# Performance work log

Measured on AMD Instinct MI355X. Metric: run time of the kernel, lower is better.

The kernel has to match this reference:

```python
import jax, jax.numpy as jnp
import numpy as np

R, N, E, IN_DIM, HID, SEM_H = 3, 50000, 500000, 256, 128, 128


def setup_inputs() -> dict:
    key = jax.random.key(0)
    ks = jax.random.split(key, 20)
    s = 0.05
    return {
        # forward tensor args
        "dst_feat": jax.random.normal(ks[0], (N, IN_DIM), jnp.float32),
        "src_feats": jax.random.normal(ks[1], (R, N, IN_DIM), jnp.float32),
        "src_idx": jax.random.randint(ks[2], (R, E), 0, N, jnp.int32),
        "dst_idx": jax.random.randint(ks[3], (R, E), 0, N, jnp.int32),
        # weight_T: per-ntype projection in_dim -> hidden (dst ntype + R src ntypes, stacked)
        "WT_dst": jax.random.normal(ks[4], (IN_DIM, HID), jnp.float32) * s,
        "bT_dst": jnp.zeros((HID,), jnp.float32),
        "WT_src": jax.random.normal(ks[5], (R, IN_DIM, HID), jnp.float32) * s,
        "bT_src": jnp.zeros((R, HID), jnp.float32),
        # GATConv params per relation (1 head, shared fc for src/dst since in_feats is int)
        "W_gat": jax.random.normal(ks[6], (R, HID, HID), jnp.float32) * s,
        "attn_l": jax.random.normal(ks[7], (R, HID), jnp.float32) * s,
        "attn_r": jax.random.normal(ks[8], (R, HID), jnp.float32) * s,
        "b_gat": jnp.zeros((R, HID), jnp.float32),
        # SemanticAttention: Linear(HID,128)+tanh+Linear(128,1,no bias)
        "W1_sem": jax.random.normal(ks[9], (HID, SEM_H), jnp.float32) * s,
        "b1_sem": jnp.zeros((SEM_H,), jnp.float32),
        "w2_sem": jax.random.normal(ks[10], (SEM_H, 1), jnp.float32) * s,
    }


def reference(dst_feat, src_feats, src_idx, dst_idx,
              WT_dst, bT_dst, WT_src, bT_src,
              W_gat, attn_l, attn_r, b_gat,
              W1_sem, b1_sem, w2_sem):
    # weight_T projections (raw feat dim != hidden_dim branch)
    h_dst = dst_feat @ WT_dst + bT_dst                                  # [N, H]
    h_src = jnp.einsum('rni,rio->rno', src_feats, WT_src) + bT_src[:, None, :]  # [R, N, H]
    n_nodes = h_dst.shape[0]

    def gat(h_s_in, si, di, W, al, ar, b):
        # DGL GATConv, 1 head, eval mode (no dropout), shared fc for src/dst
        hs = h_s_in @ W                                                 # [N, H]
        hd = h_dst @ W                                                  # [N, H]
        el = (hs * al).sum(-1)                                          # [N]
        er = (hd * ar).sum(-1)                                          # [N]
        e = el[si] + er[di]                                             # [E]
        e = jnp.where(e > 0, e, 0.2 * e)                                # leaky_relu(0.2)
        # edge softmax segmented by destination node
        m = jax.ops.segment_max(e, di, num_segments=n_nodes)
        ex = jnp.exp(e - m[di])
        ssum = jax.ops.segment_sum(ex, di, num_segments=n_nodes)
        alpha = ex / ssum[di]                                           # [E]
        out = jax.ops.segment_sum(alpha[:, None] * hs[si], di, num_segments=n_nodes)  # [N, H]
        return jax.nn.elu(out + b)                                      # activation=F.elu, + bias

    z_r = jax.vmap(gat)(h_src, src_idx, dst_idx, W_gat, attn_l, attn_r, b_gat)  # [R, N, H]

    # SemanticAttention over relations
    z_m = jnp.transpose(z_r, (1, 0, 2))                                 # [N, R, H]
    w = jnp.tanh(z_m @ W1_sem + b1_sem) @ w2_sem                        # [N, R, 1]
    a = jax.nn.softmax(w.mean(axis=0), axis=0)                          # [R, 1]
    return (z_m * a).sum(axis=1)                                        # [N, H]
```

## Files before the change

kernel.cpp:

```cpp
#include <hip/hip_runtime.h>
#include <hip/hip_bf16.h>

#define R_REL 3
#define NODE_CHUNK 512
#define BCAP 6144

typedef __attribute__((ext_vector_type(8))) short bf16x8;
typedef __attribute__((ext_vector_type(4))) float f32x4;

static inline size_t align_up(size_t x, size_t a) { return (x + a - 1) & ~(a - 1); }

__device__ __forceinline__ float eluf(float x) {
    return x > 0.f ? x : (__expf(x) - 1.f);
}
__device__ __forceinline__ unsigned short f2bf(float f) {
    __hip_bfloat16 h = __float2bfloat16(f);
    return *reinterpret_cast<unsigned short*>(&h);
}
__device__ __forceinline__ unsigned pk2bf(float lo, float hi) {
    __hip_bfloat162 h = __float22bfloat162_rn(make_float2(lo, hi));
    return *reinterpret_cast<unsigned*>(&h);
}
__device__ __forceinline__ float bf2f(unsigned short h) {
    return __uint_as_float((unsigned)h << 16);
}


__global__ void vu_kernel(const float* __restrict__ W_gat, const float* __restrict__ attn_r,
                          const float* __restrict__ WT_dst, const float* __restrict__ bT_dst,
                          float* __restrict__ u, float* __restrict__ cc) {
    int r = blockIdx.x;
    int t = threadIdx.x;
    __shared__ float ar[128];
    __shared__ float vs[128];
    if (t < 128) ar[t] = attn_r[r * 128 + t];
    __syncthreads();
    if (t < 128) {
        const float* W = W_gat + (size_t)r * 128 * 128 + (size_t)t * 128;
        float s = 0.f;
        for (int j = 0; j < 128; ++j) s += W[j] * ar[j];
        vs[t] = s;
    }
    __syncthreads();
    const float* W = WT_dst + (size_t)t * 128;
    float s = 0.f;
    for (int i = 0; i < 128; ++i) s += W[i] * vs[i];
    u[r * 256 + t] = s;
    if (t == 0) {
        float c = 0.f;
        for (int i = 0; i < 128; ++i) c += bT_dst[i] * vs[i];
        cc[r] = c;
    }
}

__global__ void wc_kernel(const float* __restrict__ WT_src, const float* __restrict__ bT_src,
                          const float* __restrict__ W_gat, float* __restrict__ Wc,
                          float* __restrict__ bc) {
    int r = blockIdx.y;
    int k = blockIdx.x;
    int j = threadIdx.x;
    __shared__ float as[128];
    const float* arow = (k < 256) ? (WT_src + ((size_t)r * 256 + k) * 128)
                                  : (bT_src + (size_t)r * 128);
    as[j] = arow[j];
    __syncthreads();
    const float* W = W_gat + (size_t)r * 128 * 128;
    float s = 0.f;
    for (int i = 0; i < 128; ++i) s += as[i] * W[(size_t)i * 128 + j];
    if (k < 256) Wc[((size_t)r * 256 + k) * 128 + j] = s;
    else         bc[(size_t)r * 128 + j] = s;
}

__global__ void pack_kernel(const float* __restrict__ S, unsigned short* __restrict__ P,
                            int relstride, int KS) {
    int r = blockIdx.y;
    int ks = blockIdx.x >> 3, cb = blockIdx.x & 7;
    int l = threadIdx.x;
    const float* Sr = S + (size_t)r * relstride;
    int col = cb * 16 + (l & 15);
    int kb = ks * 32 + (l >> 4) * 8;
    unsigned short v[8];
#pragma unroll
    for (int j = 0; j < 8; ++j) v[j] = f2bf(Sr[(size_t)(kb + j) * 128 + col]);
    unsigned short* dst = P + ((((size_t)r * KS + ks) * 8 + cb) * 64 + l) * 8;
    *(uint4*)dst = *(uint4*)v;
}


__global__ __launch_bounds__(512) void gemm_hs(
    const float* __restrict__ src, const unsigned short* __restrict__ Bpack,
    const float* __restrict__ bc, const float* __restrict__ attn_l,
    unsigned short* __restrict__ hsb, float* __restrict__ el, int N) {
    const int r = blockIdx.y;
    const int t = threadIdx.x;
    const int w = t >> 6, l = t & 63;
    __shared__ unsigned short Blds[256 * 128];

    const unsigned short* bsrc = Bpack + (size_t)r * 256 * 128;
#pragma unroll
    for (int i = 0; i < 8; ++i) {
        int c = i * 512 + t;
        *(uint4*)&Blds[(size_t)c * 8] = *(const uint4*)&bsrc[(size_t)c * 8];
    }
    __syncthreads();

    const int rowbase = blockIdx.x * 128 + w * 16;
    const int arow_i = rowbase + (l & 15);
    const int kg = l >> 4;
    const float* A = src + (size_t)r * N * 256;
    const float* arow = A + (size_t)(arow_i < N ? arow_i : N - 1) * 256;

    f32x4 acc[8] = {};
#pragma unroll
    for (int ks = 0; ks < 8; ++ks) {
        float4 a0 = *(const float4*)(arow + ks * 32 + kg * 8);
        float4 a1 = *(const float4*)(arow + ks * 32 + kg * 8 + 4);
        uint4 uv;
        uv.x = pk2bf(a0.x, a0.y);
        uv.y = pk2bf(a0.z, a0.w);
        uv.z = pk2bf(a1.x, a1.y);
        uv.w = pk2bf(a1.z, a1.w);
        bf16x8 av = *(bf16x8*)&uv;
#pragma unroll
        for (int cf = 0; cf < 8; ++cf) {
            bf16x8 bv = *(const bf16x8*)&Blds[((size_t)(ks * 8 + cf) * 64 + l) * 8];
            acc[cf] = __builtin_amdgcn_mfma_f32_16x16x32_bf16(av, bv, acc[cf], 0, 0, 0);
        }
    }
    float bcv[8], alv[8];
#pragma unroll
    for (int cf = 0; cf < 8; ++cf) {
        int col = cf * 16 + (l & 15);
        bcv[cf] = bc[r * 128 + col];
        alv[cf] = attn_l[r * 128 + col];
    }
#pragma unroll
    for (int i = 0; i < 4; ++i) {
        int row = rowbase + (l >> 4) * 4 + i;
        float pe = 0.f;
        unsigned short hv[8];
#pragma unroll
        for (int cf = 0; cf < 8; ++cf) {
            float v = acc[cf][i] + bcv[cf];
            pe += v * alv[cf];
            hv[cf] = f2bf(v);
        }
        if (row < N) {
            unsigned short* hp = hsb + ((size_t)r * N + row) * 128 + (l & 15);
#pragma unroll
            for (int cf = 0; cf < 8; ++cf) hp[cf * 16] = hv[cf];
        }
        pe += __shfl_xor(pe, 1, 64);
        pe += __shfl_xor(pe, 2, 64);
        pe += __shfl_xor(pe, 4, 64);
        pe += __shfl_xor(pe, 8, 64);
        if ((l & 15) == 0 && row < N) el[(size_t)r * N + row] = pe;
    }
}


__global__ void er_kernel(const float* __restrict__ dst_feat, const float* __restrict__ u,
                          const float* __restrict__ cc, float* __restrict__ er, int N) {
    __shared__ float us[3][256];
    for (int i = threadIdx.x; i < 3 * 256; i += 256) us[i / 256][i & 255] = u[i];
    __syncthreads();
    int wave = threadIdx.x >> 6, lane = threadIdx.x & 63;
    int n = blockIdx.x * 4 + wave;
    if (n >= N) return;
    float4 f = *(const float4*)(dst_feat + (size_t)n * 256 + lane * 4);
#pragma unroll
    for (int r = 0; r < R_REL; ++r) {
        float4 uv = *(float4*)&us[r][lane * 4];
        float s = f.x * uv.x + f.y * uv.y + f.z * uv.z + f.w * uv.w;
#pragma unroll
        for (int off = 32; off >= 1; off >>= 1) s += __shfl_xor(s, off, 64);
        if (lane == 0) er[(size_t)r * N + n] = s + cc[r];
    }
}


__global__ __launch_bounds__(256) void bucket_kernel(
    const int* __restrict__ si, const int* __restrict__ di,
    int* __restrict__ gcnt, unsigned* __restrict__ bbuf, int NB, int E) {
    const int r = blockIdx.y;
    const int t = threadIdx.x;
    const int e0 = blockIdx.x * 1024;
    __shared__ int cnt[128];
    __shared__ int base[128];
    if (t < 128) cnt[t] = 0;
    __syncthreads();
    int bk[4], rank[4]; unsigned pack[4]; bool val[4];
#pragma unroll
    for (int j = 0; j < 4; ++j) {
        int e = e0 + j * 256 + t;
        val[j] = e < E;
        bk[j] = 0; rank[j] = 0; pack[j] = 0;
        if (val[j]) {
            size_t g = (size_t)r * E + e;
            int s = si[g], d = di[g];
            bk[j] = d >> 9;
            pack[j] = (unsigned)s | ((unsigned)d << 16);
            rank[j] = atomicAdd(&cnt[bk[j]], 1);
        }
    }
    __syncthreads();
    if (t < NB && cnt[t] > 0) base[t] = atomicAdd(&gcnt[r * NB + t], cnt[t]);
    __syncthreads();
#pragma unroll
    for (int j = 0; j < 4; ++j) {
        if (val[j])
            bbuf[((size_t)r * NB + bk[j]) * BCAP + base[bk[j]] + rank[j]] = pack[j];
    }
}

__global__ __launch_bounds__(256) void hist_kernel(
    const unsigned* __restrict__ bbuf, const int* __restrict__ gcnt,
    int* __restrict__ deg, int NB, int N) {
    const int r = blockIdx.y;
    const int b = blockIdx.x;
    const int t = threadIdx.x;
    __shared__ int hist[NODE_CHUNK];
    for (int i = t; i < NODE_CHUNK; i += 256) hist[i] = 0;
    __syncthreads();
    const int cnt = gcnt[r * NB + b];
    const unsigned* bb = bbuf + ((size_t)r * NB + b) * BCAP;
    for (int i = t; i < cnt; i += 256) {
        int dloc = (bb[i] >> 16) & (NODE_CHUNK - 1);
        atomicAdd(&hist[dloc], 1);
    }
    __syncthreads();
    for (int i = t; i < NODE_CHUNK; i += 256) {
        int idx = b * NODE_CHUNK + i;
        if (idx < N) deg[(size_t)r * N + idx] = hist[i];
    }
}

__global__ __launch_bounds__(1024) void scan1_kernel(const int* __restrict__ deg,
                                                     int* __restrict__ offs,
                                                     int* __restrict__ btot, int N, int nchunk) {
    const int r = blockIdx.y;
    const int idx = blockIdx.x * 1024 + threadIdx.x;
    const int lane = threadIdx.x & 63, wave = threadIdx.x >> 6;
    __shared__ int wsum[16];
    int v = (idx < N) ? deg[(size_t)r * N + idx] : 0;
    int x = v;
#pragma unroll
    for (int off = 1; off < 64; off <<= 1) {
        int y = __shfl_up(x, off, 64);
        if (lane >= off) x += y;
    }
    if (lane == 63) wsum[wave] = x;
    __syncthreads();
    if (wave == 0 && lane < 16) {
        int y = wsum[lane];
#pragma unroll
        for (int off = 1; off < 16; off <<= 1) {
            int z = __shfl_up(y, off, 64);
            if (lane >= off) y += z;
        }
        wsum[lane] = y;
    }
    __syncthreads();
    int woff = (wave > 0) ? wsum[wave - 1] : 0;
    if (idx < N) offs[(size_t)r * N + idx] = woff + x - v;
    if (threadIdx.x == 1023) btot[r * nchunk + blockIdx.x] = woff + x;
}

__global__ __launch_bounds__(256) void scan2_kernel(const int* __restrict__ btot,
                                                    int* __restrict__ offs, int N, int nchunk) {
    const int r = blockIdx.y;
    const int chunk = blockIdx.x;
    const int t = threadIdx.x;
    const int lane = t & 63, wave = t >> 6;
    __shared__ int red[4];
    int pre = 0;
    for (int i = t; i < chunk; i += 256) pre += btot[r * nchunk + i];
#pragma unroll
    for (int off = 32; off >= 1; off >>= 1) pre += __shfl_xor(pre, off, 64);
    if (lane == 0) red[wave] = pre;
    __syncthreads();
    int ptot = red[0] + red[1] + red[2] + red[3];
    for (int j = t; j < 1024; j += 256) {
        int idx = chunk * 1024 + j;
        if (idx < N) offs[(size_t)r * N + idx] += ptot;
    }
}

__global__ __launch_bounds__(256) void fill2_kernel(
    const unsigned* __restrict__ bbuf, const int* __restrict__ gcnt,
    const int* __restrict__ offs, unsigned short* __restrict__ csr, int NB, int N, int E) {
    const int r = blockIdx.y;
    const int b = blockIdx.x;
    const int t = threadIdx.x;
    __shared__ int curl[NODE_CHUNK];
    for (int i = t; i < NODE_CHUNK; i += 256) {
        int idx = b * NODE_CHUNK + i;
        curl[i] = (idx < N) ? offs[(size_t)r * N + idx] : 0;
    }
    __syncthreads();
    const int cnt = gcnt[r * NB + b];
    const unsigned* bb = bbuf + ((size_t)r * NB + b) * BCAP;
    unsigned short* csrr = csr + (size_t)r * E;
    for (int i = t; i < cnt; i += 256) {
        unsigned pk = bb[i];
        int dloc = (pk >> 16) & (NODE_CHUNK - 1);
        int pos = atomicAdd(&curl[dloc], 1);
        csrr[pos] = (unsigned short)(pk & 0xffffu);
    }
}


__global__ __launch_bounds__(256) void gather_kernel(
    const unsigned short* __restrict__ csr, const int* __restrict__ offs,
    const int* __restrict__ deg, const float* __restrict__ el, const float* __restrict__ er,
    const unsigned short* __restrict__ hsb, const float* __restrict__ b_gat,
    unsigned short* __restrict__ z, int N, int E) {
    const int r = blockIdx.y;
    const int t = threadIdx.x;
    const int gid = t >> 4;
    const int gl = t & 15;
    const int d = blockIdx.x * 16 + gid;
    if (d >= N) return;
    const int beg = offs[(size_t)r * N + d];
    const int dg = deg[(size_t)r * N + d];
    float ac[8] = {0.f, 0.f, 0.f, 0.f, 0.f, 0.f, 0.f, 0.f};
    float ssum = 0.f;
    const float erd = er[(size_t)r * N + d];
    const float* elr = el + (size_t)r * N;
    const unsigned short* csrr = csr + (size_t)r * E;
    const unsigned short* hsr = hsb + (size_t)r * N * 128;
    for (int i = beg; i < beg + dg; ++i) {
        int src = csrr[i];
        float e = elr[src] + erd;
        e = e > 0.f ? e : 0.2f * e;
        float p = __expf(e);
        ssum += p;
        uint4 hw = *(const uint4*)(hsr + (size_t)src * 128 + gl * 8);
        ac[0] += p * bf2f((unsigned short)(hw.x & 0xffffu));
        ac[1] += p * bf2f((unsigned short)(hw.x >> 16));
        ac[2] += p * bf2f((unsigned short)(hw.y & 0xffffu));
        ac[3] += p * bf2f((unsigned short)(hw.y >> 16));
        ac[4] += p * bf2f((unsigned short)(hw.z & 0xffffu));
        ac[5] += p * bf2f((unsigned short)(hw.z >> 16));
        ac[6] += p * bf2f((unsigned short)(hw.w & 0xffffu));
        ac[7] += p * bf2f((unsigned short)(hw.w >> 16));
    }
    float inv = (dg > 0) ? 1.f / ssum : 0.f;
    const float* bg = b_gat + r * 128 + gl * 8;
    uint4 ow;
    ow.x = pk2bf(eluf(ac[0] * inv + bg[0]), eluf(ac[1] * inv + bg[1]));
    ow.y = pk2bf(eluf(ac[2] * inv + bg[2]), eluf(ac[3] * inv + bg[3]));
    ow.z = pk2bf(eluf(ac[4] * inv + bg[4]), eluf(ac[5] * inv + bg[5]));
    ow.w = pk2bf(eluf(ac[6] * inv + bg[6]), eluf(ac[7] * inv + bg[7]));
    *(uint4*)(z + ((size_t)r * N + d) * 128 + gl * 8) = ow;
}


__global__ __launch_bounds__(256) void gemm_sem(
    const unsigned short* __restrict__ z, const unsigned short* __restrict__ W1p,
    const float* __restrict__ b1, const float* __restrict__ w2,
    float* __restrict__ wpart, int N) {
    const int r = blockIdx.y;
    const int n0 = blockIdx.x * 64;
    const int t = threadIdx.x;
    const int w = t >> 6, l = t & 63;
    __shared__ unsigned short Alds[64 * 128];
    __shared__ float sred[4];
    const unsigned short* A = z + (size_t)r * N * 128;
#pragma unroll
    for (int i = 0; i < 4; ++i) {
        int cid = t + 256 * i;
        int row = cid >> 4, kc = cid & 15;
        uint4 v = make_uint4(0, 0, 0, 0);
        if (n0 + row < N) v = *(const uint4*)(A + (size_t)(n0 + row) * 128 + kc * 8);
        int off = ((row * 256) + kc * 16) ^ ((row & 7) << 4);
        *(uint4*)((char*)Alds + off) = v;
    }
    __syncthreads();

    const bf16x8* bp = (const bf16x8*)W1p;
    f32x4 acc[8] = {};
    const int arow = w * 16 + (l & 15);
#pragma unroll
    for (int ks = 0; ks < 4; ++ks) {
        int aoff = ((arow * 256) + ks * 64 + (l >> 4) * 16) ^ ((arow & 7) << 4);
        bf16x8 av = *(const bf16x8*)((char*)Alds + aoff);
#pragma unroll
        for (int cf = 0; cf < 8; ++cf) {
            bf16x8 bv = bp[(ks * 8 + cf) * 64 + l];
            acc[cf] = __builtin_amdgcn_mfma_f32_16x16x32_bf16(av, bv, acc[cf], 0, 0, 0);
        }
    }
    float b1v[8], w2v[8];
#pragma unroll
    for (int cf = 0; cf < 8; ++cf) {
        int col = cf * 16 + (l & 15);
        b1v[cf] = b1[col];
        w2v[cf] = w2[col];
    }
    float wloc = 0.f;
#pragma unroll
    for (int i = 0; i < 4; ++i) {
        int row = n0 + w * 16 + (l >> 4) * 4 + i;
        float s = 0.f;
#pragma unroll
        for (int cf = 0; cf < 8; ++cf) s += tanhf(acc[cf][i] + b1v[cf]) * w2v[cf];
        s += __shfl_xor(s, 1, 64);
        s += __shfl_xor(s, 2, 64);
        s += __shfl_xor(s, 4, 64);
        s += __shfl_xor(s, 8, 64);
        if ((l & 15) == 0 && row < N) wloc += s;
    }
    wloc += __shfl_xor(wloc, 16, 64);
    wloc += __shfl_xor(wloc, 32, 64);
    if (l == 0) sred[w] = wloc;
    __syncthreads();
    if (t == 0)
        wpart[(size_t)r * gridDim.x + blockIdx.x] = sred[0] + sred[1] + sred[2] + sred[3];
}


__global__ void reduce_sem(const float* __restrict__ wpart, float* __restrict__ aw,
                           int nblk, int N) {
    const int t = threadIdx.x, l = t & 63, w = t >> 6;
    __shared__ float sred[R_REL][4];
    float s[R_REL] = {0.f, 0.f, 0.f};
    for (int i = t; i < nblk; i += 256) {
#pragma unroll
        for (int r = 0; r < R_REL; ++r) s[r] += wpart[(size_t)r * nblk + i];
    }
#pragma unroll
    for (int r = 0; r < R_REL; ++r) {
#pragma unroll
        for (int off = 32; off >= 1; off >>= 1) s[r] += __shfl_xor(s[r], off, 64);
        if (l == 0) sred[r][w] = s[r];
    }
    __syncthreads();
    if (t == 0) {
        float w0 = (sred[0][0] + sred[0][1] + sred[0][2] + sred[0][3]) / (float)N;
        float w1 = (sred[1][0] + sred[1][1] + sred[1][2] + sred[1][3]) / (float)N;
        float w2 = (sred[2][0] + sred[2][1] + sred[2][2] + sred[2][3]) / (float)N;
        float m = fmaxf(w0, fmaxf(w1, w2));
        float e0 = __expf(w0 - m), e1 = __expf(w1 - m), e2 = __expf(w2 - m);
        float si = e0 + e1 + e2;
        aw[0] = e0 / si; aw[1] = e1 / si; aw[2] = e2 / si;
    }
}

__global__ void combine(const unsigned short* __restrict__ z, const float* __restrict__ aw,
                        float* __restrict__ out, int N) {
    int idx = blockIdx.x * 256 + threadIdx.x;
    if (idx >= N * 32) return;
    int n = idx >> 5, c4 = idx & 31;
    float a0 = aw[0], a1 = aw[1], a2 = aw[2];
    uint2 z0 = *(const uint2*)(z + ((size_t)0 * N + n) * 128 + c4 * 4);
    uint2 z1 = *(const uint2*)(z + ((size_t)1 * N + n) * 128 + c4 * 4);
    uint2 z2 = *(const uint2*)(z + ((size_t)2 * N + n) * 128 + c4 * 4);
    float4 o;
    o.x = a0 * bf2f((unsigned short)(z0.x & 0xffffu)) + a1 * bf2f((unsigned short)(z1.x & 0xffffu)) + a2 * bf2f((unsigned short)(z2.x & 0xffffu));
    o.y = a0 * bf2f((unsigned short)(z0.x >> 16))     + a1 * bf2f((unsigned short)(z1.x >> 16))     + a2 * bf2f((unsigned short)(z2.x >> 16));
    o.z = a0 * bf2f((unsigned short)(z0.y & 0xffffu)) + a1 * bf2f((unsigned short)(z1.y & 0xffffu)) + a2 * bf2f((unsigned short)(z2.y & 0xffffu));
    o.w = a0 * bf2f((unsigned short)(z0.y >> 16))     + a1 * bf2f((unsigned short)(z1.y >> 16))     + a2 * bf2f((unsigned short)(z2.y >> 16));
    *(float4*)(out + (size_t)idx * 4) = o;
}


extern "C" void kernel_launch(void* const* d_in, const int* in_sizes, int n_in,
                              void* d_out, int out_size, void* d_ws, size_t ws_size,
                              hipStream_t stream) {
    const float* dst_feat = (const float*)d_in[0];
    const float* src_feats = (const float*)d_in[1];
    const int*   src_idx  = (const int*)d_in[2];
    const int*   dst_idx  = (const int*)d_in[3];
    const float* WT_dst   = (const float*)d_in[4];
    const float* bT_dst   = (const float*)d_in[5];
    const float* WT_src   = (const float*)d_in[6];
    const float* bT_src   = (const float*)d_in[7];
    const float* W_gat    = (const float*)d_in[8];
    const float* attn_l   = (const float*)d_in[9];
    const float* attn_r   = (const float*)d_in[10];
    const float* b_gat    = (const float*)d_in[11];
    const float* W1_sem   = (const float*)d_in[12];
    const float* b1_sem   = (const float*)d_in[13];
    const float* w2_sem   = (const float*)d_in[14];

    const int N = in_sizes[0] / 256;
    const int E = in_sizes[2] / R_REL;
    float* out = (float*)d_out;

    const int nblk = (N + 63) / 64;
    const int nblk_hs = (N + 127) / 128;
    const int nchunk = (N + 1023) / 1024;
    const int NB = (N + NODE_CHUNK - 1) / NODE_CHUNK;

    char* ws = (char*)d_ws;
    size_t off = 0;
    auto alloc = [&](size_t bytes) { char* p = ws + off; off = align_up(off + bytes, 256); return p; };
    unsigned short* hsb   = (unsigned short*)alloc((size_t)R_REL * N * 128 * 2);
    unsigned short* zbuf  = (unsigned short*)alloc((size_t)R_REL * N * 128 * 2);
    float*    Wc    = (float*)alloc((size_t)R_REL * 256 * 128 * 4);
    unsigned short* Wcp   = (unsigned short*)alloc((size_t)R_REL * 256 * 128 * 2);
    unsigned short* W1p   = (unsigned short*)alloc((size_t)128 * 128 * 2);
    float*    bc    = (float*)alloc(R_REL * 128 * 4);
    float*    u     = (float*)alloc(R_REL * 256 * 4);
    float*    cc    = (float*)alloc(R_REL * 4);
    float*    el    = (float*)alloc((size_t)R_REL * N * 4);
    float*    er    = (float*)alloc((size_t)R_REL * N * 4);
    int*      deg   = (int*)alloc((size_t)R_REL * N * 4);
    int*      offs  = (int*)alloc((size_t)R_REL * N * 4);
    int*      btot  = (int*)alloc((size_t)R_REL * nchunk * 4);
    int*      gcnt  = (int*)alloc((size_t)R_REL * NB * 4);
    unsigned* bbuf  = (unsigned*)alloc((size_t)R_REL * NB * BCAP * 4);
    unsigned short* csr = (unsigned short*)alloc((size_t)R_REL * E * 2);
    float*    wpart = (float*)alloc((size_t)R_REL * nblk * 4);
    float*    aw    = (float*)alloc(R_REL * 4);

    hipMemsetAsync(gcnt, 0, (size_t)R_REL * NB * 4, stream);

    vu_kernel<<<R_REL, 256, 0, stream>>>(W_gat, attn_r, WT_dst, bT_dst, u, cc);
    wc_kernel<<<dim3(257, R_REL), 128, 0, stream>>>(WT_src, bT_src, W_gat, Wc, bc);
    pack_kernel<<<dim3(64, R_REL), 64, 0, stream>>>(Wc, Wcp, 256 * 128, 8);
    pack_kernel<<<dim3(32, 1), 64, 0, stream>>>(W1_sem, W1p, 0, 4);

    bucket_kernel<<<dim3((E + 1023) / 1024, R_REL), 256, 0, stream>>>(src_idx, dst_idx, gcnt, bbuf, NB, E);
    hist_kernel<<<dim3(NB, R_REL), 256, 0, stream>>>(bbuf, gcnt, deg, NB, N);
    scan1_kernel<<<dim3(nchunk, R_REL), 1024, 0, stream>>>(deg, offs, btot, N, nchunk);
    scan2_kernel<<<dim3(nchunk, R_REL), 256, 0, stream>>>(btot, offs, N, nchunk);
    fill2_kernel<<<dim3(NB, R_REL), 256, 0, stream>>>(bbuf, gcnt, offs, csr, NB, N, E);

    gemm_hs<<<dim3(nblk_hs, R_REL), 512, 0, stream>>>(src_feats, Wcp, bc, attn_l, hsb, el, N);
    er_kernel<<<(N + 3) / 4, 256, 0, stream>>>(dst_feat, u, cc, er, N);

    gather_kernel<<<dim3((N + 15) / 16, R_REL), 256, 0, stream>>>(csr, offs, deg, el, er, hsb, b_gat, zbuf, N, E);

    gemm_sem<<<dim3(nblk, R_REL), 256, 0, stream>>>(zbuf, W1p, b1_sem, w2_sem, wpart, N);
    reduce_sem<<<1, 256, 0, stream>>>(wpart, aw, nblk, N);
    combine<<<(N * 32 + 255) / 256, 256, 0, stream>>>(zbuf, aw, out, N);
}
```

Baseline: 252.0 us.

## Precompute edge attention weights during CSR fill and unroll gather by four

```diff
diff --git a/kernel.cpp b/kernel.cpp
--- a/kernel.cpp
+++ b/kernel.cpp
@@ -286,35 +286,42 @@
     }
 }
 
-__global__ __launch_bounds__(256) void fill2_kernel(
+__global__ __launch_bounds__(256) void fill2p_kernel(
     const unsigned* __restrict__ bbuf, const int* __restrict__ gcnt,
-    const int* __restrict__ offs, unsigned short* __restrict__ csr, int NB, int N, int E) {
+    const int* __restrict__ offs, const float* __restrict__ el, const float* __restrict__ er,
+    uint2* __restrict__ epair, int NB, int N, int E) {
     const int r = blockIdx.y;
     const int b = blockIdx.x;
     const int t = threadIdx.x;
     __shared__ int curl[NODE_CHUNK];
+    __shared__ float erl[NODE_CHUNK];
     for (int i = t; i < NODE_CHUNK; i += 256) {
         int idx = b * NODE_CHUNK + i;
         curl[i] = (idx < N) ? offs[(size_t)r * N + idx] : 0;
+        erl[i]  = (idx < N) ? er[(size_t)r * N + idx] : 0.f;
     }
     __syncthreads();
     const int cnt = gcnt[r * NB + b];
     const unsigned* bb = bbuf + ((size_t)r * NB + b) * BCAP;
-    unsigned short* csrr = csr + (size_t)r * E;
+    const float* elr = el + (size_t)r * N;
+    uint2* epr = epair + (size_t)r * E;
     for (int i = t; i < cnt; i += 256) {
         unsigned pk = bb[i];
+        int src = pk & 0xffffu;
         int dloc = (pk >> 16) & (NODE_CHUNK - 1);
+        float e = elr[src] + erl[dloc];
+        e = e > 0.f ? e : 0.2f * e;
+        float p = __expf(e);
         int pos = atomicAdd(&curl[dloc], 1);
-        csrr[pos] = (unsigned short)(pk & 0xffffu);
+        epr[pos] = make_uint2((unsigned)src, __float_as_uint(p));
     }
 }
 
 
 __global__ __launch_bounds__(256) void gather_kernel(
-    const unsigned short* __restrict__ csr, const int* __restrict__ offs,
-    const int* __restrict__ deg, const float* __restrict__ el, const float* __restrict__ er,
-    const unsigned short* __restrict__ hsb, const float* __restrict__ b_gat,
-    unsigned short* __restrict__ z, int N, int E) {
+    const uint2* __restrict__ epair, const int* __restrict__ offs,
+    const int* __restrict__ deg, const unsigned short* __restrict__ hsb,
+    const float* __restrict__ b_gat, unsigned short* __restrict__ z, int N, int E) {
     const int r = blockIdx.y;
     const int t = threadIdx.x;
     const int gid = t >> 4;
@@ -325,17 +332,41 @@
     const int dg = deg[(size_t)r * N + d];
     float ac[8] = {0.f, 0.f, 0.f, 0.f, 0.f, 0.f, 0.f, 0.f};
     float ssum = 0.f;
-    const float erd = er[(size_t)r * N + d];
-    const float* elr = el + (size_t)r * N;
-    const unsigned short* csrr = csr + (size_t)r * E;
+    const uint2* epr = epair + (size_t)r * E;
     const unsigned short* hsr = hsb + (size_t)r * N * 128;
-    for (int i = beg; i < beg + dg; ++i) {
-        int src = csrr[i];
-        float e = elr[src] + erd;
-        e = e > 0.f ? e : 0.2f * e;
-        float p = __expf(e);
+    int i = beg;
+    const int end = beg + dg;
+    for (; i + 3 < end; i += 4) {
+        uint2 v0 = epr[i], v1 = epr[i + 1], v2 = epr[i + 2], v3 = epr[i + 3];
+        uint4 h0 = *(const uint4*)(hsr + (size_t)v0.x * 128 + gl * 8);
+        uint4 h1 = *(const uint4*)(hsr + (size_t)v1.x * 128 + gl * 8);
+        uint4 h2 = *(const uint4*)(hsr + (size_t)v2.x * 128 + gl * 8);
+        uint4 h3 = *(const uint4*)(hsr + (size_t)v3.x * 128 + gl * 8);
+        float p0 = __uint_as_float(v0.y), p1 = __uint_as_float(v1.y);
+        float p2 = __uint_as_float(v2.y), p3 = __uint_as_float(v3.y);
+        ssum += p0 + p1 + p2 + p3;
+        ac[0] += p0 * bf2f((unsigned short)(h0.x & 0xffffu)) + p1 * bf2f((unsigned short)(h1.x & 0xffffu))
+               + p2 * bf2f((unsigned short)(h2.x & 0xffffu)) + p3 * bf2f((unsigned short)(h3.x & 0xffffu));
+        ac[1] += p0 * bf2f((unsigned short)(h0.x >> 16)) + p1 * bf2f((unsigned short)(h1.x >> 16))
+               + p2 * bf2f((unsigned short)(h2.x >> 16)) + p3 * bf2f((unsigned short)(h3.x >> 16));
+        ac[2] += p0 * bf2f((unsigned short)(h0.y & 0xffffu)) + p1 * bf2f((unsigned short)(h1.y & 0xffffu))
+               + p2 * bf2f((unsigned short)(h2.y & 0xffffu)) + p3 * bf2f((unsigned short)(h3.y & 0xffffu));
+        ac[3] += p0 * bf2f((unsigned short)(h0.y >> 16)) + p1 * bf2f((unsigned short)(h1.y >> 16))
+               + p2 * bf2f((unsigned short)(h2.y >> 16)) + p3 * bf2f((unsigned short)(h3.y >> 16));
+        ac[4] += p0 * bf2f((unsigned short)(h0.z & 0xffffu)) + p1 * bf2f((unsigned short)(h1.z & 0xffffu))
+               + p2 * bf2f((unsigned short)(h2.z & 0xffffu)) + p3 * bf2f((unsigned short)(h3.z & 0xffffu));
+        ac[5] += p0 * bf2f((unsigned short)(h0.z >> 16)) + p1 * bf2f((unsigned short)(h1.z >> 16))
+               + p2 * bf2f((unsigned short)(h2.z >> 16)) + p3 * bf2f((unsigned short)(h3.z >> 16));
+        ac[6] += p0 * bf2f((unsigned short)(h0.w & 0xffffu)) + p1 * bf2f((unsigned short)(h1.w & 0xffffu))
+               + p2 * bf2f((unsigned short)(h2.w & 0xffffu)) + p3 * bf2f((unsigned short)(h3.w & 0xffffu));
+        ac[7] += p0 * bf2f((unsigned short)(h0.w >> 16)) + p1 * bf2f((unsigned short)(h1.w >> 16))
+               + p2 * bf2f((unsigned short)(h2.w >> 16)) + p3 * bf2f((unsigned short)(h3.w >> 16));
+    }
+    for (; i < end; ++i) {
+        uint2 v = epr[i];
+        float p = __uint_as_float(v.y);
         ssum += p;
-        uint4 hw = *(const uint4*)(hsr + (size_t)src * 128 + gl * 8);
+        uint4 hw = *(const uint4*)(hsr + (size_t)v.x * 128 + gl * 8);
         ac[0] += p * bf2f((unsigned short)(hw.x & 0xffffu));
         ac[1] += p * bf2f((unsigned short)(hw.x >> 16));
         ac[2] += p * bf2f((unsigned short)(hw.y & 0xffffu));
@@ -511,7 +542,7 @@
     int*      btot  = (int*)alloc((size_t)R_REL * nchunk * 4);
     int*      gcnt  = (int*)alloc((size_t)R_REL * NB * 4);
     unsigned* bbuf  = (unsigned*)alloc((size_t)R_REL * NB * BCAP * 4);
-    unsigned short* csr = (unsigned short*)alloc((size_t)R_REL * E * 2);
+    uint2*    epair = (uint2*)alloc((size_t)R_REL * E * 8);
     float*    wpart = (float*)alloc((size_t)R_REL * nblk * 4);
     float*    aw    = (float*)alloc(R_REL * 4);
 
@@ -522,16 +553,16 @@
     pack_kernel<<<dim3(64, R_REL), 64, 0, stream>>>(Wc, Wcp, 256 * 128, 8);
     pack_kernel<<<dim3(32, 1), 64, 0, stream>>>(W1_sem, W1p, 0, 4);
 
+    gemm_hs<<<dim3(nblk_hs, R_REL), 512, 0, stream>>>(src_feats, Wcp, bc, attn_l, hsb, el, N);
+    er_kernel<<<(N + 3) / 4, 256, 0, stream>>>(dst_feat, u, cc, er, N);
+
     bucket_kernel<<<dim3((E + 1023) / 1024, R_REL), 256, 0, stream>>>(src_idx, dst_idx, gcnt, bbuf, NB, E);
     hist_kernel<<<dim3(NB, R_REL), 256, 0, stream>>>(bbuf, gcnt, deg, NB, N);
     scan1_kernel<<<dim3(nchunk, R_REL), 1024, 0, stream>>>(deg, offs, btot, N, nchunk);
     scan2_kernel<<<dim3(nchunk, R_REL), 256, 0, stream>>>(btot, offs, N, nchunk);
-    fill2_kernel<<<dim3(NB, R_REL), 256, 0, stream>>>(bbuf, gcnt, offs, csr, NB, N, E);
-
-    gemm_hs<<<dim3(nblk_hs, R_REL), 512, 0, stream>>>(src_feats, Wcp, bc, attn_l, hsb, el, N);
-    er_kernel<<<(N + 3) / 4, 256, 0, stream>>>(dst_feat, u, cc, er, N);
-
-    gather_kernel<<<dim3((N + 15) / 16, R_REL), 256, 0, stream>>>(csr, offs, deg, el, er, hsb, b_gat, zbuf, N, E);
+    fill2p_kernel<<<dim3(NB, R_REL), 256, 0, stream>>>(bbuf, gcnt, offs, el, er, epair, NB, N, E);
+
+    gather_kernel<<<dim3((N + 15) / 16, R_REL), 256, 0, stream>>>(epair, offs, deg, hsb, b_gat, zbuf, N, E);
 
     gemm_sem<<<dim3(nblk, R_REL), 256, 0, stream>>>(zbuf, W1p, b1_sem, w2_sem, wpart, N);
     reduce_sem<<<1, 256, 0, stream>>>(wpart, aw, nblk, N);
```

Measured after the change: 247.4 us. No clear change (-1.8%).
